# Optimization experiments

Measured on AMD Instinct MI355X. Metric: run time of the kernel, lower is better.

Reference implementation:

```python
import jax, jax.numpy as jnp
import numpy as np

H = 8  # n_heads (init_kwarg, closed over)


def setup_inputs() -> dict:
    key = jax.random.key(0)
    ks = jax.random.split(key, 5)
    B, T, D, L = 8, 4096, 512, 128
    # lecun_normal: std = 1/sqrt(fan_in), fan_in = first dim here
    X = jax.random.normal(ks[0], (B, T, D), dtype=jnp.float32)
    Wk = jax.random.normal(ks[1], (D, L), dtype=jnp.float32) / np.sqrt(D)
    Wq = jax.random.normal(ks[2], (D, L), dtype=jnp.float32) / np.sqrt(D)
    Wv = jax.random.normal(ks[3], (D, D), dtype=jnp.float32) / np.sqrt(D)
    o_proj = jax.random.normal(ks[4], (D, D), dtype=jnp.float32) / np.sqrt(D)
    return {"X": X, "Wk": Wk, "Wq": Wq, "Wv": Wv, "o_proj": o_proj}


def reference(X, Wk, Wq, Wv, o_proj):
    B, T, D = X.shape
    L = Wk.shape[1]
    Dh, Lh = D // H, L // H
    # time-major projections: (T, B, H, *)
    V = jnp.einsum('DM,BTD->TBM', Wv, X).reshape(T, B, H, Dh)
    Q = jnp.einsum('DL,BTD->TBL', Wq, X).reshape(T, B, H, Lh)
    K = jnp.einsum('DL,BTD->TBL', Wk, X).reshape(T, B, H, Lh)
    scale = jax.lax.rsqrt(jnp.array(Dh, dtype=jnp.float32))
    K_exp = jnp.exp(K * scale)                      # (T,B,H,Lh)
    alpha = jnp.cumsum(K_exp, axis=0)               # causal normalizer
    Qs = jax.nn.softmax(Q * scale, axis=-1) / alpha # (T,B,H,Lh)

    def step(carry, args):
        qs_t, ke_t, v_t = args
        carry = carry + jnp.einsum('bhl,bhd->bhld', ke_t, v_t)
        y_t = jnp.einsum('bhl,bhld->bhd', qs_t, carry)
        return carry, y_t

    init = jnp.zeros((B, H, Lh, Dh), dtype=X.dtype)
    _, y = jax.lax.scan(step, init, (Qs, K_exp, V), unroll=16)  # y: (T,B,H,Dh)
    # faithful to source: transpose(3,0,1,2) then reshape(B,T,D)
    y = y.transpose(3, 0, 1, 2).reshape(B, T, D)
    return y @ o_proj
```

## Files before the change

kernel.cpp:

```cpp
#include <hip/hip_runtime.h>
#include <hip/hip_bf16.h>

#define B_ 8
#define T_ 4096
#define D_ 512
#define L_ 128
#define H_ 8
#define Dh_ 64
#define Lh_ 16
#define M_ (B_*T_)
#define SCALE 0.125f

typedef __bf16 v8bf __attribute__((ext_vector_type(8)));
typedef float  v4f  __attribute__((ext_vector_type(4)));
typedef unsigned short u16;
typedef u16 v8u __attribute__((ext_vector_type(8)));

__device__ __forceinline__ float b2f(u16 h){
    unsigned int u = ((unsigned int)h) << 16;
    return __builtin_bit_cast(float, u);
}
__device__ __forceinline__ u16 f2bf(float f){
    unsigned int u = __builtin_bit_cast(unsigned int, f);
    u += 0x7FFFu + ((u >> 16) & 1u);
    return (u16)(u >> 16);
}

__device__ __forceinline__ void wave_fence() {
    asm volatile("" ::: "memory");
}

__device__ __forceinline__ void gload16(const u16* g, u16* l) {
    __builtin_amdgcn_global_load_lds(
        (const __attribute__((address_space(1))) unsigned int*)(g),
        (__attribute__((address_space(3))) unsigned int*)(l), 16, 0, 0);
}

__global__ __launch_bounds__(256) void prep(
        const float* __restrict__ X,  const float* __restrict__ Wq,
        const float* __restrict__ Wk, const float* __restrict__ Wv,
        const float* __restrict__ Wo,
        u16* __restrict__ Xb, u16* __restrict__ WT, u16* __restrict__ OT)
{
    int bid = blockIdx.x;
    if (bid < 8192) {
        const size_t i = (size_t)bid * 256 + threadIdx.x;
        const float4* s = (const float4*)X + i * 2;
        float4 a = s[0], b = s[1];
        v8u o;
        o[0] = f2bf(a.x); o[1] = f2bf(a.y); o[2] = f2bf(a.z); o[3] = f2bf(a.w);
        o[4] = f2bf(b.x); o[5] = f2bf(b.y); o[6] = f2bf(b.z); o[7] = f2bf(b.w);
        *((v8u*)Xb + i) = o;
        return;
    }
    bid -= 8192;
    const float* src; u16* dst; int cols, bx, by;
    if (bid < 64)       { src = Wq; dst = WT;             cols = 128; bx = bid & 3;  by = bid >> 2; }
    else if (bid < 128) { src = Wk; dst = WT + 128 * 512; cols = 128; bid -= 64;  bx = bid & 3;  by = bid >> 2; }
    else if (bid < 384) { src = Wv; dst = WT + 256 * 512; cols = 512; bid -= 128; bx = bid & 15; by = bid >> 4; }
    else                { src = Wo; dst = OT;             cols = 512; bid -= 384; bx = bid & 15; by = bid >> 4; }
    __shared__ u16 tile[32][33];
    const int tx = threadIdx.x & 31, ty = threadIdx.x >> 5;
    const int c0 = bx * 32, r0 = by * 32;
    #pragma unroll
    for (int i = 0; i < 32; i += 8)
        tile[ty + i][tx] = f2bf(src[(size_t)(r0 + ty + i) * cols + c0 + tx]);
    __syncthreads();
    #pragma unroll
    for (int i = 0; i < 32; i += 8)
        dst[(size_t)(c0 + ty + i) * 512 + r0 + tx] = tile[tx][ty + i];
}

template<int MODE, int NY>
__global__ __launch_bounds__(256) void gemm_mfma(
        const u16* __restrict__ A, const u16* __restrict__ Bt,
        float* __restrict__ Qo, u16* __restrict__ KEo,
        u16* __restrict__ Vo, float* __restrict__ OutF)
{
    __shared__ __align__(16) u16 As[128 * 64];
    __shared__ __align__(16) u16 Bs[128 * 64];
    const int tid  = threadIdx.x;
    const int wave = tid >> 6, lane = tid & 63;
    const int wm = wave >> 1, wn = wave & 1;
    const int lm = lane & 15, quad = lane >> 4;

    const int bid = blockIdx.x;
    const int xcd = bid & 7, j = bid >> 3;
    const int grp = j / (8 * NY), r = j % (8 * NY);
    const int by  = r >> 3, pin = r & 7;
    const int bx  = xcd * 32 + grp * 8 + pin;
    const int gm0 = bx * 128, gn0 = by * 128;

    const int srow0 = wave * 32 + (lane >> 3);
    const int sg    = lane & 7;

    v4f acc[4][4];
    #pragma unroll
    for (int i = 0; i < 4; i++)
        #pragma unroll
        for (int j2 = 0; j2 < 4; j2++)
            acc[i][j2] = (v4f){0.f, 0.f, 0.f, 0.f};

    for (int kt = 0; kt < 8; ++kt) {
        const int k0 = kt * 64;
        #pragma unroll
        for (int rr = 0; rr < 4; ++rr) {
            const int row = srow0 + rr * 8;
            const int col = ((sg ^ (row & 7)) << 3) + k0;
            gload16(&A [(size_t)(gm0 + row) * 512 + col], &As[(wave * 4 + rr) * 512]);
            gload16(&Bt[(size_t)(gn0 + row) * 512 + col], &Bs[(wave * 4 + rr) * 512]);
        }
        __syncthreads();
        v8bf af[2][4], bfr[2][4];
        #pragma unroll
        for (int ks = 0; ks < 2; ks++)
            #pragma unroll
            for (int mi = 0; mi < 4; mi++) {
                const int g  = ks * 4 + quad;
                const int ra = wm * 64 + mi * 16 + lm;
                const int rb = wn * 64 + mi * 16 + lm;
                af [ks][mi] = *(const v8bf*)&As[ra * 64 + ((g ^ (ra & 7)) << 3)];
                bfr[ks][mi] = *(const v8bf*)&Bs[rb * 64 + ((g ^ (rb & 7)) << 3)];
            }
        #pragma unroll
        for (int ks = 0; ks < 2; ks++)
            #pragma unroll
            for (int mi = 0; mi < 4; mi++)
                #pragma unroll
                for (int ni = 0; ni < 4; ni++)
                    acc[mi][ni] = __builtin_amdgcn_mfma_f32_16x16x32_bf16(
                                      af[ks][mi], bfr[ks][ni], acc[mi][ni], 0, 0, 0);
        __syncthreads();
    }

    if (MODE == 1) {
        #pragma unroll
        for (int mi = 0; mi < 4; mi++)
          #pragma unroll
          for (int ni = 0; ni < 4; ni++)
            #pragma unroll
            for (int i = 0; i < 4; i++) {
                int row = gm0 + wm * 64 + mi * 16 + quad * 4 + i;
                int col = gn0 + wn * 64 + ni * 16 + lm;
                OutF[(size_t)row * 512 + col] = acc[mi][ni][i];
            }
    } else if (gn0 == 0) {
        #pragma unroll
        for (int mi = 0; mi < 4; mi++)
          #pragma unroll
          for (int ni = 0; ni < 4; ni++)
            #pragma unroll
            for (int i = 0; i < 4; i++) {
                int row = gm0 + wm * 64 + mi * 16 + quad * 4 + i;
                int col = wn * 64 + ni * 16 + lm;
                float qv = acc[mi][ni][i] * SCALE;
                float m = qv;
                #pragma unroll
                for (int off = 1; off < 16; off <<= 1) m = fmaxf(m, __shfl_xor(m, off));
                float e = __expf(qv - m);
                float s = e;
                #pragma unroll
                for (int off = 1; off < 16; off <<= 1) s += __shfl_xor(s, off);
                Qo[(size_t)row * 128 + col] = e / s;
            }
    } else if (gn0 == 128) {
        #pragma unroll
        for (int mi = 0; mi < 4; mi++)
          #pragma unroll
          for (int ni = 0; ni < 4; ni++)
            #pragma unroll
            for (int i = 0; i < 4; i++) {
                int row = gm0 + wm * 64 + mi * 16 + quad * 4 + i;
                int col = wn * 64 + ni * 16 + lm;
                KEo[(size_t)row * 128 + col] = f2bf(__expf(acc[mi][ni][i] * SCALE));
            }
    } else {
        #pragma unroll
        for (int mi = 0; mi < 4; mi++)
          #pragma unroll
          for (int ni = 0; ni < 4; ni++)
            #pragma unroll
            for (int i = 0; i < 4; i++) {
                int row = gm0 + wm * 64 + mi * 16 + quad * 4 + i;
                int col = gn0 + wn * 64 + ni * 16 + lm - 256;
                Vo[(size_t)row * 512 + col] = f2bf(acc[mi][ni][i]);
            }
    }
}

__global__ __launch_bounds__(256, 2) void chunk_sums_mfma(
        const u16* __restrict__ KE, const u16* __restrict__ V,
        float* __restrict__ Mc, float* __restrict__ AB)
{
    struct CLDS { u16 KA[16][72]; u16 VT[64][72]; };
    __shared__ __align__(16) CLDS lds[4];
    const int tid = threadIdx.x, wave = tid >> 6, lane = tid & 63;
    const int lm = lane & 15, quad = lane >> 4;
    const int ch = blockIdx.x * 4 + wave;
    const int bh = ch >> 6, c = ch & 63, b = bh >> 3, h = bh & 7;
    const int t0 = b * T_ + c * 64;
    CLDS& L = lds[wave];

    {
        const u16* kp = KE + (size_t)(t0 + lane) * L_ + h * Lh_;
        v8u k0 = *(const v8u*)kp, k1 = *(const v8u*)(kp + 8);
        #pragma unroll
        for (int l = 0; l < 8; l++) L.KA[l][lane]     = k0[l];
        #pragma unroll
        for (int l = 0; l < 8; l++) L.KA[l + 8][lane] = k1[l];
        const u16* vp = V + (size_t)(t0 + lane) * D_ + h * Dh_;
        #pragma unroll
        for (int seg = 0; seg < 8; ++seg) {
            v8u pv = *(const v8u*)(vp + seg * 8);
            #pragma unroll
            for (int j = 0; j < 8; j++) L.VT[seg * 8 + j][lane] = pv[j];
        }
    }
    wave_fence();

    v8bf ka[2];
    #pragma unroll
    for (int ki = 0; ki < 2; ki++)
        ka[ki] = *(const v8bf*)&L.KA[lm][ki * 32 + quad * 8];

    v8u onesu;
    #pragma unroll
    for (int j = 0; j < 8; j++) onesu[j] = 0x3F80;
    v8bf ones = __builtin_bit_cast(v8bf, onesu);

    v4f accL = (v4f){0.f, 0.f, 0.f, 0.f};
    accL = __builtin_amdgcn_mfma_f32_16x16x32_bf16(ka[0], ones, accL, 0, 0, 0);
    accL = __builtin_amdgcn_mfma_f32_16x16x32_bf16(ka[1], ones, accL, 0, 0, 0);

    v4f accM[4];
    #pragma unroll
    for (int nd = 0; nd < 4; nd++) accM[nd] = (v4f){0.f, 0.f, 0.f, 0.f};
    #pragma unroll
    for (int nd = 0; nd < 4; nd++)
        #pragma unroll
        for (int ki = 0; ki < 2; ki++) {
            v8bf vb = *(const v8bf*)&L.VT[nd * 16 + lm][ki * 32 + quad * 8];
            accM[nd] = __builtin_amdgcn_mfma_f32_16x16x32_bf16(ka[ki], vb, accM[nd], 0, 0, 0);
        }

    float* mcb = Mc + (size_t)ch * 1024;
    #pragma unroll
    for (int nd = 0; nd < 4; nd++)
        #pragma unroll
        for (int i = 0; i < 4; i++)
            mcb[(quad * 4 + i) * 64 + nd * 16 + lm] = accM[nd][i];
    if (lm == 0) {
        #pragma unroll
        for (int i = 0; i < 4; i++) AB[ch * 16 + quad * 4 + i] = accL[i];
    }
}

__global__ __launch_bounds__(256) void chunk_prefix(
        const float* __restrict__ Mc, u16* __restrict__ McB,
        float* __restrict__ AB)
{
    const int bh = blockIdx.x >> 2, qq = blockIdx.x & 3;
    const int i = qq * 256 + threadIdx.x;
    const size_t base = (size_t)bh * 64 * 1024 + i;
    float v[64];
    #pragma unroll
    for (int c = 0; c < 64; ++c) v[c] = Mc[base + (size_t)c * 1024];
    float run = 0.f;
    #pragma unroll
    for (int c = 0; c < 64; ++c) {
        McB[base + (size_t)c * 1024] = f2bf(run);
        run += v[c];
    }
    if (qq == 0 && threadIdx.x < 16) {
        const int l = threadIdx.x;
        float a[64];
        #pragma unroll
        for (int c = 0; c < 64; ++c) a[c] = AB[(bh * 64 + c) * 16 + l];
        float r2 = 0.f;
        #pragma unroll
        for (int c = 0; c < 64; ++c) {
            AB[(bh * 64 + c) * 16 + l] = r2;
            r2 += a[c];
        }
    }
}

__global__ __launch_bounds__(256, 2) void intra_mfma(
        const float* __restrict__ QS, const u16* __restrict__ KE,
        const u16* __restrict__ V, const u16* __restrict__ McB,
        const float* __restrict__ AB, u16* __restrict__ Y)
{
    struct ILDS {
        union {
            struct { u16 KA[16][72]; u16 Sc[16][72]; u16 qs[64][40]; } s;
            u16 p[64][72];
        } r;
        u16 VT[64][72];
    };
    __shared__ __align__(16) ILDS lds[4];
    const int tid = threadIdx.x, wave = tid >> 6, lane = tid & 63;
    const int lm = lane & 15, quad = lane >> 4;
    const int ch = blockIdx.x * 4 + wave;
    const int bh = ch >> 6, c = ch & 63, b = bh >> 3, h = bh & 7;
    const int t0 = b * T_ + c * 64;
    ILDS& L = lds[wave];

    {
        const u16* kp = KE + (size_t)(t0 + lane) * L_ + h * Lh_;
        v8u k0 = *(const v8u*)kp, k1 = *(const v8u*)(kp + 8);
        #pragma unroll
        for (int l = 0; l < 8; l++) L.r.s.KA[l][lane]     = k0[l];
        #pragma unroll
        for (int l = 0; l < 8; l++) L.r.s.KA[l + 8][lane] = k1[l];
        const u16* vp = V + (size_t)(t0 + lane) * D_ + h * Dh_;
        #pragma unroll
        for (int seg = 0; seg < 8; ++seg) {
            v8u pv = *(const v8u*)(vp + seg * 8);
            #pragma unroll
            for (int j = 0; j < 8; j++) L.VT[seg * 8 + j][lane] = pv[j];
        }
        const u16* mcb = McB + (size_t)ch * 1024;
        #pragma unroll
        for (int l = 0; l < 16; l++)
            L.r.s.Sc[l][lane] = mcb[l * 64 + lane];
        v8u z8;
        #pragma unroll
        for (int j = 0; j < 8; j++) z8[j] = 0;
        *(v8u*)&L.r.s.qs[lane][16] = z8;
        *(v8u*)&L.r.s.qs[lane][24] = z8;
    }
    const float ab = AB[ch * 16 + lm];
    wave_fence();

    v4f acc_a[4];
    #pragma unroll
    for (int mi = 0; mi < 4; mi++) acc_a[mi] = (v4f){ab, ab, ab, ab};
    #pragma unroll
    for (int mi = 0; mi < 4; mi++)
        #pragma unroll
        for (int ki = 0; ki < 2; ki++) {
            if (ki == 1 && mi < 2) continue;
            v8u ta;
            #pragma unroll
            for (int j = 0; j < 8; j++)
                ta[j] = (ki * 32 + quad * 8 + j <= mi * 16 + lm) ? (u16)0x3F80 : (u16)0;
            v8bf kb = *(const v8bf*)&L.r.s.KA[lm][ki * 32 + quad * 8];
            acc_a[mi] = __builtin_amdgcn_mfma_f32_16x16x32_bf16(
                            __builtin_bit_cast(v8bf, ta), kb, acc_a[mi], 0, 0, 0);
        }

    #pragma unroll
    for (int mi = 0; mi < 4; mi++)
        #pragma unroll
        for (int i = 0; i < 4; i++) {
            int t = mi * 16 + quad * 4 + i;
            float qs = QS[(size_t)(t0 + t) * L_ + h * Lh_ + lm];
            L.r.s.qs[t][lm] = f2bf(qs / acc_a[mi][i]);
        }
    wave_fence();

    v8bf aq[4];
    #pragma unroll
    for (int mi = 0; mi < 4; mi++)
        aq[mi] = *(const v8bf*)&L.r.s.qs[mi * 16 + lm][quad * 8];

    v4f accP[4][4], accY[4][4];
    #pragma unroll
    for (int mi = 0; mi < 4; mi++)
        #pragma unroll
        for (int ni = 0; ni < 4; ni++) {
            accP[mi][ni] = (v4f){0.f, 0.f, 0.f, 0.f};
            accY[mi][ni] = (v4f){0.f, 0.f, 0.f, 0.f};
        }

    #pragma unroll
    for (int ni = 0; ni < 4; ni++) {
        v8u kbu;
        #pragma unroll
        for (int j = 0; j < 8; j++) kbu[j] = 0;
        if (quad < 2) {
            #pragma unroll
            for (int j = 0; j < 8; j++)
                kbu[j] = L.r.s.KA[quad * 8 + j][ni * 16 + lm];
        }
        v8bf kbf = __builtin_bit_cast(v8bf, kbu);
        #pragma unroll
        for (int mi = ni; mi < 4; mi++)
            accP[mi][ni] = __builtin_amdgcn_mfma_f32_16x16x32_bf16(
                               aq[mi], kbf, accP[mi][ni], 0, 0, 0);
    }
    #pragma unroll
    for (int nd = 0; nd < 4; nd++) {
        v8u scu;
        #pragma unroll
        for (int j = 0; j < 8; j++) scu[j] = 0;
        if (quad < 2) {
            #pragma unroll
            for (int j = 0; j < 8; j++)
                scu[j] = L.r.s.Sc[quad * 8 + j][nd * 16 + lm];
        }
        v8bf scf = __builtin_bit_cast(v8bf, scu);
        #pragma unroll
        for (int mi = 0; mi < 4; mi++)
            accY[mi][nd] = __builtin_amdgcn_mfma_f32_16x16x32_bf16(
                               aq[mi], scf, accY[mi][nd], 0, 0, 0);
    }
    wave_fence();

    #pragma unroll
    for (int mi = 0; mi < 4; mi++)
        #pragma unroll
        for (int ni = 0; ni < 4; ni++)
            #pragma unroll
            for (int i = 0; i < 4; i++) {
                int t = mi * 16 + quad * 4 + i, tp = ni * 16 + lm;
                float pv = (ni < mi) ? accP[mi][ni][i]
                          : (ni == mi ? ((tp <= t) ? accP[mi][ni][i] : 0.f) : 0.f);
                L.r.p[t][tp] = f2bf(pv);
            }
    wave_fence();

    v8bf vb[4][2];
    #pragma unroll
    for (int nd = 0; nd < 4; nd++)
        #pragma unroll
        for (int ki = 0; ki < 2; ki++)
            vb[nd][ki] = *(const v8bf*)&L.VT[nd * 16 + lm][ki * 32 + quad * 8];
    #pragma unroll
    for (int mi = 0; mi < 4; mi++)
        #pragma unroll
        for (int ki = 0; ki < 2; ki++) {
            if (ki == 1 && mi < 2) continue;
            v8bf pa = *(const v8bf*)&L.r.p[mi * 16 + lm][ki * 32 + quad * 8];
            #pragma unroll
            for (int nd = 0; nd < 4; nd++)
                accY[mi][nd] = __builtin_amdgcn_mfma_f32_16x16x32_bf16(
                                   pa, vb[nd][ki], accY[mi][nd], 0, 0, 0);
        }

    #pragma unroll
    for (int mi = 0; mi < 4; mi++)
        #pragma unroll
        for (int nd = 0; nd < 4; nd++)
            #pragma unroll
            for (int i = 0; i < 4; i++) {
                int t = mi * 16 + quad * 4 + i;
                Y[(((size_t)(c * 64 + t)) * 64 + bh) * 64 + nd * 16 + lm] =
                    f2bf(accY[mi][nd][i]);
            }
}

__global__ __launch_bounds__(256) void transpose_Y(
        const u16* __restrict__ Y, u16* __restrict__ Z)
{
    __shared__ __align__(16) u16 tile[4][64][72];
    const int wave = threadIdx.x >> 6, t = threadIdx.x & 63;
    const int g = blockIdx.x * 4 + wave;
    u16 (*tl)[72] = tile[wave];
    const u16* yp = Y + (size_t)(g * 64 + t) * 64;
    #pragma unroll
    for (int seg = 0; seg < 8; ++seg)
        *(v8u*)&tl[t][seg * 8] = *(const v8u*)(yp + seg * 8);
    wave_fence();
    const int cl = t & 7, dq = t >> 3;
    #pragma unroll
    for (int p = 0; p < 8; ++p) {
        const int dh = p * 8 + dq;
        v8u pk;
        #pragma unroll
        for (int j = 0; j < 8; j++) pk[j] = tl[cl * 8 + j][dh];
        *(v8u*)&Z[(size_t)dh * 262144 + (size_t)g * 64 + cl * 8] = pk;
    }
}

extern "C" void kernel_launch(void* const* d_in, const int* in_sizes, int n_in,
                              void* d_out, int out_size, void* d_ws, size_t ws_size,
                              hipStream_t stream)
{
    (void)in_sizes; (void)n_in; (void)out_size; (void)ws_size;
    const float* X  = (const float*)d_in[0];
    const float* Wk = (const float*)d_in[1];
    const float* Wq = (const float*)d_in[2];
    const float* Wv = (const float*)d_in[3];
    const float* Wo = (const float*)d_in[4];
    float* Out = (float*)d_out;

    char* p = (char*)d_ws;
    auto alloc = [&](size_t bytes) { char* r = p; p += (bytes + 255) & ~(size_t)255; return r; };
    u16*   Xb = (u16*)  alloc((size_t)M_ * 512 * 2);
    u16*   WT = (u16*)  alloc((size_t)768 * 512 * 2);
    u16*   OT = (u16*)  alloc((size_t)512 * 512 * 2);
    u16*   V  = (u16*)  alloc((size_t)M_ * 512 * 2);
    float* Mc = (float*)alloc((size_t)4096 * 1024 * 4);
    float* AB = (float*)alloc((size_t)4096 * 16 * 4);
    float* Q  = (float*)alloc((size_t)M_ * 128 * 4);
    u16*   KE = (u16*)  alloc((size_t)M_ * 128 * 2);
    u16*   Y  = (u16*)  alloc((size_t)M_ * 512 * 2);
    u16*   Z  = (u16*)Mc;
    u16*   McB = (u16*)Xb;

    prep<<<8832, 256, 0, stream>>>(X, Wq, Wk, Wv, Wo, Xb, WT, OT);

    gemm_mfma<0, 6><<<1536, 256, 0, stream>>>(Xb, WT, Q, KE, V, nullptr);
    chunk_sums_mfma<<<1024, 256, 0, stream>>>(KE, V, Mc, AB);
    chunk_prefix   <<<256,  256, 0, stream>>>(Mc, McB, AB);
    intra_mfma     <<<1024, 256, 0, stream>>>(Q, KE, V, McB, AB, Y);
    transpose_Y    <<<1024, 256, 0, stream>>>(Y, Z);
    gemm_mfma<1, 4><<<1024, 256, 0, stream>>>(Z, OT, nullptr, nullptr, nullptr, Out);
}
```

Measured before the change: 248.5 us.

## Widen GEMM tiles to 128x256 with 8 waves, store Q as bf16, fix transpose LDS pattern

Both projection GEMMs now use 512-thread blocks computing 128x256 output tiles, so each A tile is loaded once for twice as many columns and the grid is halved. The softmaxed Q is written as bf16 instead of fp32, halving its write and read traffic in the intra kernel at some precision cost. transpose_Y now scatters into LDS on write and reads contiguous 16-byte vectors, replacing the strided gather on read. The larger blocks raise LDS use and register pressure per block, and the launch_bounds occupancy hint may constrain register allocation.

```diff
diff --git a/kernel.cpp b/kernel.cpp
--- a/kernel.cpp
+++ b/kernel.cpp
@@ -72,16 +72,16 @@
 }
 
 template<int MODE, int NY>
-__global__ __launch_bounds__(256) void gemm_mfma(
+__global__ __launch_bounds__(512, 6) void gemm_mfma(
         const u16* __restrict__ A, const u16* __restrict__ Bt,
-        float* __restrict__ Qo, u16* __restrict__ KEo,
+        u16* __restrict__ Qo, u16* __restrict__ KEo,
         u16* __restrict__ Vo, float* __restrict__ OutF)
 {
     __shared__ __align__(16) u16 As[128 * 64];
-    __shared__ __align__(16) u16 Bs[128 * 64];
+    __shared__ __align__(16) u16 Bs[256 * 64];
     const int tid  = threadIdx.x;
     const int wave = tid >> 6, lane = tid & 63;
-    const int wm = wave >> 1, wn = wave & 1;
+    const int wm = wave >> 2, wn = wave & 3;
     const int lm = lane & 15, quad = lane >> 4;
 
     const int bid = blockIdx.x;
@@ -89,10 +89,10 @@
     const int grp = j / (8 * NY), r = j % (8 * NY);
     const int by  = r >> 3, pin = r & 7;
     const int bx  = xcd * 32 + grp * 8 + pin;
-    const int gm0 = bx * 128, gn0 = by * 128;
-
-    const int srow0 = wave * 32 + (lane >> 3);
-    const int sg    = lane & 7;
+    const int gm0 = bx * 128, gn0 = by * 256;
+
+    const int sg   = lane & 7;
+    const int lrow = lane >> 3;
 
     v4f acc[4][4];
     #pragma unroll
@@ -104,11 +104,16 @@
     for (int kt = 0; kt < 8; ++kt) {
         const int k0 = kt * 64;
         #pragma unroll
-        for (int rr = 0; rr < 4; ++rr) {
-            const int row = srow0 + rr * 8;
+        for (int a = 0; a < 2; ++a) {
+            const int row = wave * 16 + a * 8 + lrow;
             const int col = ((sg ^ (row & 7)) << 3) + k0;
-            gload16(&A [(size_t)(gm0 + row) * 512 + col], &As[(wave * 4 + rr) * 512]);
-            gload16(&Bt[(size_t)(gn0 + row) * 512 + col], &Bs[(wave * 4 + rr) * 512]);
+            gload16(&A[(size_t)(gm0 + row) * 512 + col], &As[(wave * 16 + a * 8) * 64]);
+        }
+        #pragma unroll
+        for (int b = 0; b < 4; ++b) {
+            const int row = wave * 32 + b * 8 + lrow;
+            const int col = ((sg ^ (row & 7)) << 3) + k0;
+            gload16(&Bt[(size_t)(gn0 + row) * 512 + col], &Bs[(wave * 32 + b * 8) * 64]);
         }
         __syncthreads();
         v8bf af[2][4], bfr[2][4];
@@ -145,35 +150,37 @@
                 OutF[(size_t)row * 512 + col] = acc[mi][ni][i];
             }
     } else if (gn0 == 0) {
-        #pragma unroll
-        for (int mi = 0; mi < 4; mi++)
-          #pragma unroll
-          for (int ni = 0; ni < 4; ni++)
-            #pragma unroll
-            for (int i = 0; i < 4; i++) {
-                int row = gm0 + wm * 64 + mi * 16 + quad * 4 + i;
-                int col = wn * 64 + ni * 16 + lm;
-                float qv = acc[mi][ni][i] * SCALE;
-                float m = qv;
+        if (wn < 2) {
+            #pragma unroll
+            for (int mi = 0; mi < 4; mi++)
+              #pragma unroll
+              for (int ni = 0; ni < 4; ni++)
                 #pragma unroll
-                for (int off = 1; off < 16; off <<= 1) m = fmaxf(m, __shfl_xor(m, off));
-                float e = __expf(qv - m);
-                float s = e;
+                for (int i = 0; i < 4; i++) {
+                    int row = gm0 + wm * 64 + mi * 16 + quad * 4 + i;
+                    int col = wn * 64 + ni * 16 + lm;
+                    float qv = acc[mi][ni][i] * SCALE;
+                    float m = qv;
+                    #pragma unroll
+                    for (int off = 1; off < 16; off <<= 1) m = fmaxf(m, __shfl_xor(m, off));
+                    float e = __expf(qv - m);
+                    float s = e;
+                    #pragma unroll
+                    for (int off = 1; off < 16; off <<= 1) s += __shfl_xor(s, off);
+                    Qo[(size_t)row * 128 + col] = f2bf(e / s);
+                }
+        } else {
+            #pragma unroll
+            for (int mi = 0; mi < 4; mi++)
+              #pragma unroll
+              for (int ni = 0; ni < 4; ni++)
                 #pragma unroll
-                for (int off = 1; off < 16; off <<= 1) s += __shfl_xor(s, off);
-                Qo[(size_t)row * 128 + col] = e / s;
-            }
-    } else if (gn0 == 128) {
-        #pragma unroll
-        for (int mi = 0; mi < 4; mi++)
-          #pragma unroll
-          for (int ni = 0; ni < 4; ni++)
-            #pragma unroll
-            for (int i = 0; i < 4; i++) {
-                int row = gm0 + wm * 64 + mi * 16 + quad * 4 + i;
-                int col = wn * 64 + ni * 16 + lm;
-                KEo[(size_t)row * 128 + col] = f2bf(__expf(acc[mi][ni][i] * SCALE));
-            }
+                for (int i = 0; i < 4; i++) {
+                    int row = gm0 + wm * 64 + mi * 16 + quad * 4 + i;
+                    int col = (wn - 2) * 64 + ni * 16 + lm;
+                    KEo[(size_t)row * 128 + col] = f2bf(__expf(acc[mi][ni][i] * SCALE));
+                }
+        }
     } else {
         #pragma unroll
         for (int mi = 0; mi < 4; mi++)
@@ -286,7 +293,7 @@
 }
 
 __global__ __launch_bounds__(256, 2) void intra_mfma(
-        const float* __restrict__ QS, const u16* __restrict__ KE,
+        const u16* __restrict__ QS, const u16* __restrict__ KE,
         const u16* __restrict__ V, const u16* __restrict__ McB,
         const float* __restrict__ AB, u16* __restrict__ Y)
 {
@@ -354,7 +361,7 @@
         #pragma unroll
         for (int i = 0; i < 4; i++) {
             int t = mi * 16 + quad * 4 + i;
-            float qs = QS[(size_t)(t0 + t) * L_ + h * Lh_ + lm];
+            float qs = b2f(QS[(size_t)(t0 + t) * L_ + h * Lh_ + lm]);
             L.r.s.qs[t][lm] = f2bf(qs / acc_a[mi][i]);
         }
     wave_fence();
@@ -459,16 +466,17 @@
     u16 (*tl)[72] = tile[wave];
     const u16* yp = Y + (size_t)(g * 64 + t) * 64;
     #pragma unroll
-    for (int seg = 0; seg < 8; ++seg)
-        *(v8u*)&tl[t][seg * 8] = *(const v8u*)(yp + seg * 8);
+    for (int seg = 0; seg < 8; ++seg) {
+        v8u v = *(const v8u*)(yp + seg * 8);
+        #pragma unroll
+        for (int j = 0; j < 8; j++) tl[seg * 8 + j][t] = v[j];
+    }
     wave_fence();
     const int cl = t & 7, dq = t >> 3;
     #pragma unroll
     for (int p = 0; p < 8; ++p) {
         const int dh = p * 8 + dq;
-        v8u pk;
-        #pragma unroll
-        for (int j = 0; j < 8; j++) pk[j] = tl[cl * 8 + j][dh];
+        v8u pk = *(const v8u*)&tl[dh][cl * 8];
         *(v8u*)&Z[(size_t)dh * 262144 + (size_t)g * 64 + cl * 8] = pk;
     }
 }
@@ -493,7 +501,7 @@
     u16*   V  = (u16*)  alloc((size_t)M_ * 512 * 2);
     float* Mc = (float*)alloc((size_t)4096 * 1024 * 4);
     float* AB = (float*)alloc((size_t)4096 * 16 * 4);
-    float* Q  = (float*)alloc((size_t)M_ * 128 * 4);
+    u16*   Q  = (u16*)  alloc((size_t)M_ * 128 * 2);
     u16*   KE = (u16*)  alloc((size_t)M_ * 128 * 2);
     u16*   Y  = (u16*)  alloc((size_t)M_ * 512 * 2);
     u16*   Z  = (u16*)Mc;
@@ -501,10 +509,10 @@
 
     prep<<<8832, 256, 0, stream>>>(X, Wq, Wk, Wv, Wo, Xb, WT, OT);
 
-    gemm_mfma<0, 6><<<1536, 256, 0, stream>>>(Xb, WT, Q, KE, V, nullptr);
+    gemm_mfma<0, 3><<<768, 512, 0, stream>>>(Xb, WT, Q, KE, V, nullptr);
     chunk_sums_mfma<<<1024, 256, 0, stream>>>(KE, V, Mc, AB);
     chunk_prefix   <<<256,  256, 0, stream>>>(Mc, McB, AB);
     intra_mfma     <<<1024, 256, 0, stream>>>(Q, KE, V, McB, AB, Y);
     transpose_Y    <<<1024, 256, 0, stream>>>(Y, Z);
-    gemm_mfma<1, 4><<<1024, 256, 0, stream>>>(Z, OT, nullptr, nullptr, nullptr, Out);
-}
+    gemm_mfma<1, 2><<<512, 512, 0, stream>>>(Z, OT, nullptr, nullptr, nullptr, Out);
+}
```

After: 550.8 us. 122% more time.
